# Kernel optimization log

Measured on AMD Instinct MI355X. Metric: run time of the kernel, lower is better.

Reference implementation:

```python
import jax, jax.numpy as jnp
import numpy as np

OUT, IN, GS = 4096, 4096, 128

def setup_inputs() -> dict:
    key = jax.random.key(0)
    k1, k2, k3 = jax.random.split(key, 3)
    x = jax.random.normal(k1, (2, 4096, IN), dtype=jnp.float32)
    # ternary codes in {-1, 0, 1}, stored as int8
    ternary = (jax.random.randint(k2, (OUT, IN), 0, 3) - 1).astype(jnp.int8)
    # per-group positive scales (one per contiguous group of GS weights)
    n_groups = OUT * IN // GS
    scales = jax.random.uniform(k3, (n_groups,), dtype=jnp.float32, minval=0.01, maxval=0.1)
    return {"x": x, "ternary": ternary, "scales": scales}

def reference(x, ternary, scales):
    # Reconstruct fp32 weight: each group of GS flattened weights shares one scale.
    w = (ternary.astype(jnp.float32).reshape(-1, GS) * scales[:, None]).reshape(OUT, IN)
    # F.linear: x @ W^T
    return jnp.einsum('bsi,oi->bso', x, w)
```

## Files before the change

### kernel.cpp

```cpp
#include <hip/hip_runtime.h>
#include <hip/hip_bf16.h>


#define M_DIM 8192
#define N_DIM 4096
#define K_DIM 4096
#define NGRP 32

#define BM 256
#define BN 256
#define NT 64
#define SLOT_B 16384
#define TILE_B 32768
#define A_BYTES (32ull * NT * TILE_B)
#define B_BYTES (16ull * NT * TILE_B)
#define A_CHUNKS (32 * 64 * 2 * 1024)
#define B_CHUNKS (16 * 64 * 2 * 1024)

typedef float f32x4 __attribute__((ext_vector_type(4)));
typedef float f32x16 __attribute__((ext_vector_type(16)));
typedef short bf16x8 __attribute__((ext_vector_type(8)));

__device__ __forceinline__ unsigned bfpack(unsigned lo, unsigned hi) {
  lo = (lo + 0x7FFFu + ((lo >> 16) & 1u)) >> 16;
  hi = (hi + 0x7FFFu + ((hi >> 16) & 1u)) & 0xFFFF0000u;
  return lo | hi;
}

__global__ void prep_ab(const float* __restrict__ X, const int* __restrict__ T,
                        const float* __restrict__ S, char* __restrict__ A,
                        char* __restrict__ B) {
  const int idx0 = blockIdx.x * blockDim.x + threadIdx.x;
  const int stride = gridDim.x * blockDim.x;
  for (int c = idx0; c < A_CHUNKS; c += stride) {
    int w = c & 1023, slot = c >> 10;
    int s = w >> 8, r = w & 255;
    int kk = slot & 1, kt = (slot >> 1) & 63, bm = slot >> 7;
    int gr = bm * 256 + r;
    int k0 = kt * 64 + kk * 32 + s * 8;
    const uint4* p = reinterpret_cast<const uint4*>(X + (size_t)gr * K_DIM + k0);
    uint4 u = p[0], v = p[1];
    uint4 o;
    o.x = bfpack(u.x, u.y);
    o.y = bfpack(u.z, u.w);
    o.z = bfpack(v.x, v.y);
    o.w = bfpack(v.z, v.w);
    *reinterpret_cast<uint4*>(A + (size_t)c * 16) = o;
  }
  for (int c = idx0; c < B_CHUNKS; c += stride) {
    int w = c & 1023, slot = c >> 10;
    int s = w >> 8, r = w & 255;
    int kk = slot & 1, kt = (slot >> 1) & 63, bn = slot >> 7;
    int gn = bn * 256 + r;
    int k0 = kt * 64 + kk * 32 + s * 8;
    unsigned su = __builtin_bit_cast(unsigned, S[(size_t)gn * NGRP + (kt >> 1)]);
    unsigned sb = (su + 0x7FFFu + ((su >> 16) & 1u)) >> 16;
    const int4* p = reinterpret_cast<const int4*>(T + (size_t)gn * K_DIM + k0);
    int4 u = p[0], v = p[1];
    int t0[8] = {u.x, u.y, u.z, u.w, v.x, v.y, v.z, v.w};
    unsigned h[8];
#pragma unroll
    for (int e = 0; e < 8; ++e) {
      unsigned sgn = ((unsigned)(t0[e] >> 31)) & 0x8000u;
      h[e] = t0[e] ? (sb | sgn) : 0u;
    }
    uint4 o;
    o.x = h[0] | (h[1] << 16);
    o.y = h[2] | (h[3] << 16);
    o.z = h[4] | (h[5] << 16);
    o.w = h[6] | (h[7] << 16);
    *reinterpret_cast<uint4*>(B + (size_t)c * 16) = o;
  }
}

__device__ __forceinline__ void gload16(const char* g, const char* l) {
  __builtin_amdgcn_global_load_lds(
      (const __attribute__((address_space(1))) void*)g,
      (__attribute__((address_space(3))) void*)l, 16, 0, 0);
}

__global__ __launch_bounds__(512, 2) void dqt_gemm32(
    const char* __restrict__ Aws, const char* __restrict__ Bws,
    float* __restrict__ C) {
  __shared__ __align__(16) char lds[131072];

  int b = blockIdx.x;
  int xcd = b & 7, idx = b >> 3;
  int bm = xcd * 4 + (idx >> 4);
  int bn = idx & 15;

  const int tid = threadIdx.x;
  const int lane = tid & 63;
  const int wid = tid >> 6;
  const int wr = wid >> 2;
  const int wc = wid & 3;
  const int l31 = lane & 31;
  const int lh = lane >> 5;

  const char* pA = Aws + ((size_t)bm << 21) + wid * 2048 + lane * 16;
  const char* pB = Bws + ((size_t)bn << 21) + wid * 2048 + lane * 16;
  const int sbase = wid * 2048;

#define STAGE(dstoff, src)                                \
  do {                                                    \
    gload16((src), lds + (dstoff) + sbase);               \
    gload16((src) + 1024, lds + (dstoff) + sbase + 1024); \
  } while (0)

  const int aoff = lh * 4096 + (wr * 128 + l31) * 16;
  const int boff = 32768 + lh * 4096 + (wc * 64 + l31) * 16;

  f32x16 acc[4][2] = {};

  STAGE(0, pA);
  STAGE(16384, pA + 16384);
  STAGE(32768, pB);
  STAGE(49152, pB + 16384);
  STAGE(65536, pA + 32768);
  STAGE(65536 + 32768, pB + 32768);
  asm volatile("s_waitcnt vmcnt(4)" ::: "memory");
  __builtin_amdgcn_s_barrier();

#pragma unroll 1
  for (int t = 0; t < NT; ++t) {
    const int cb = (t & 1) << 16;
    const int nb = (~t & 1) << 16;
    const char* sA1 = pA + (t + 1) * TILE_B;
    const char* sB1 = pB + (t + 1) * TILE_B;
    const char* sA2 = pA + (t + 2) * TILE_B;
    const char* sB2 = pB + (t + 2) * TILE_B;
    bf16x8 af[4], bq[2];

#pragma unroll
    for (int m = 0; m < 4; ++m)
      af[m] = *(const bf16x8*)(lds + cb + 0 + aoff + m * 512);
#pragma unroll
    for (int n = 0; n < 2; ++n)
      bq[n] = *(const bf16x8*)(lds + cb + 0 + boff + n * 512);
    if (t + 1 < NT) {
      STAGE(nb + 16384, sA1 + 16384);
      STAGE(nb + 49152, sB1 + 16384);
    }
    __builtin_amdgcn_s_barrier();
    __builtin_amdgcn_s_setprio(1);
#pragma unroll
    for (int m = 0; m < 4; ++m)
#pragma unroll
      for (int n = 0; n < 2; ++n)
        acc[m][n] = __builtin_amdgcn_mfma_f32_32x32x16_bf16(af[m], bq[n], acc[m][n], 0, 0, 0);
    __builtin_amdgcn_s_setprio(0);
    __builtin_amdgcn_s_barrier();

#pragma unroll
    for (int m = 0; m < 4; ++m)
      af[m] = *(const bf16x8*)(lds + cb + 8192 + aoff + m * 512);
#pragma unroll
    for (int n = 0; n < 2; ++n)
      bq[n] = *(const bf16x8*)(lds + cb + 8192 + boff + n * 512);
    __builtin_amdgcn_s_barrier();
    __builtin_amdgcn_s_setprio(1);
#pragma unroll
    for (int m = 0; m < 4; ++m)
#pragma unroll
      for (int n = 0; n < 2; ++n)
        acc[m][n] = __builtin_amdgcn_mfma_f32_32x32x16_bf16(af[m], bq[n], acc[m][n], 0, 0, 0);
    __builtin_amdgcn_s_setprio(0);
    __builtin_amdgcn_s_barrier();

#pragma unroll
    for (int m = 0; m < 4; ++m)
      af[m] = *(const bf16x8*)(lds + cb + 16384 + aoff + m * 512);
#pragma unroll
    for (int n = 0; n < 2; ++n)
      bq[n] = *(const bf16x8*)(lds + cb + 16384 + boff + n * 512);
    if (t + 2 < NT) STAGE(cb + 0, sA2);
    __builtin_amdgcn_s_barrier();
    __builtin_amdgcn_s_setprio(1);
#pragma unroll
    for (int m = 0; m < 4; ++m)
#pragma unroll
      for (int n = 0; n < 2; ++n)
        acc[m][n] = __builtin_amdgcn_mfma_f32_32x32x16_bf16(af[m], bq[n], acc[m][n], 0, 0, 0);
    __builtin_amdgcn_s_setprio(0);
    __builtin_amdgcn_s_barrier();

#pragma unroll
    for (int m = 0; m < 4; ++m)
      af[m] = *(const bf16x8*)(lds + cb + 16384 + 8192 + aoff + m * 512);
#pragma unroll
    for (int n = 0; n < 2; ++n)
      bq[n] = *(const bf16x8*)(lds + cb + 16384 + 8192 + boff + n * 512);
    if (t + 2 < NT) STAGE(cb + 32768, sB2);
    __builtin_amdgcn_s_barrier();
    __builtin_amdgcn_s_setprio(1);
#pragma unroll
    for (int m = 0; m < 4; ++m)
#pragma unroll
      for (int n = 0; n < 2; ++n)
        acc[m][n] = __builtin_amdgcn_mfma_f32_32x32x16_bf16(af[m], bq[n], acc[m][n], 0, 0, 0);
    __builtin_amdgcn_s_setprio(0);
    if (t < NT - 3)
      asm volatile("s_waitcnt vmcnt(4)" ::: "memory");
    else
      asm volatile("s_waitcnt vmcnt(0)" ::: "memory");
    __builtin_amdgcn_s_barrier();
  }

  const int row0 = bm * BM + wr * 128 + 4 * lh;
  const int col0 = bn * BN + wc * 64 + l31;
#pragma unroll
  for (int m = 0; m < 4; ++m)
#pragma unroll
    for (int n = 0; n < 2; ++n) {
      float* cp = C + (size_t)(row0 + m * 32) * N_DIM + col0 + n * 32;
#pragma unroll
      for (int q = 0; q < 16; ++q)
        cp[(size_t)((q & 3) + 8 * (q >> 2)) * N_DIM] = acc[m][n][q];
    }
#undef STAGE
}

struct StageRegs { float4 a0, a1, a2, a3; int4 b0, b1, b2, b3; float s; };

__device__ __forceinline__ void fb_issue(StageRegs& r, const float* __restrict__ X,
    const int* __restrict__ T, const float* __restrict__ S,
    int arow_g, int brow_g, int kt, int kq) {
  const int kbase = kt * 64;
  const float4* pa = reinterpret_cast<const float4*>(X + (size_t)arow_g * K_DIM + kbase + kq * 16);
  r.a0 = pa[0]; r.a1 = pa[1]; r.a2 = pa[2]; r.a3 = pa[3];
  const int4* pb = reinterpret_cast<const int4*>(T + (size_t)brow_g * K_DIM + kbase + kq * 16);
  r.b0 = pb[0]; r.b1 = pb[1]; r.b2 = pb[2]; r.b3 = pb[3];
  r.s = S[(size_t)brow_g * NGRP + (kt >> 1)];
}
__device__ __forceinline__ void fb_stage(const StageRegs& r, char* als, char* bls,
                                         int rrow, int kq) {
  const int xorv = (rrow & 7) << 4;
  const int base = rrow * 128 + kq * 32;
  const float* xf = (const float*)&r.a0;
  const int* wi = (const int*)&r.b0;
  bf16x8 av0, av1, wv0, wv1;
#pragma unroll
  for (int e = 0; e < 8; ++e) {
    av0[e] = __builtin_bit_cast(short, __float2bfloat16(xf[e]));
    av1[e] = __builtin_bit_cast(short, __float2bfloat16(xf[8 + e]));
    wv0[e] = __builtin_bit_cast(short, __float2bfloat16((float)wi[e] * r.s));
    wv1[e] = __builtin_bit_cast(short, __float2bfloat16((float)wi[8 + e] * r.s));
  }
  *(bf16x8*)(als + ((base) ^ xorv)) = av0;
  *(bf16x8*)(als + ((base + 16) ^ xorv)) = av1;
  *(bf16x8*)(bls + ((base) ^ xorv)) = wv0;
  *(bf16x8*)(bls + ((base + 16) ^ xorv)) = wv1;
}
__device__ __forceinline__ void fb_compute(const char* als, const char* bls,
    int lane, int wr, int wc, f32x4 (&acc)[4][2]) {
  const int lm = lane & 15;
  const int lk = (lane >> 4) << 4;
  const int xorv = (lm & 7) << 4;
#pragma unroll
  for (int ks = 0; ks < 2; ++ks) {
    const int kb = ks * 64 + lk;
    bf16x8 ah[4], bq[2];
#pragma unroll
    for (int i = 0; i < 4; ++i)
      ah[i] = *(const bf16x8*)(als + (((wr * 64 + i * 16 + lm) * 128 + kb) ^ xorv));
#pragma unroll
    for (int j = 0; j < 2; ++j)
      bq[j] = *(const bf16x8*)(bls + (((wc * 32 + j * 16 + lm) * 128 + kb) ^ xorv));
#pragma unroll
    for (int i = 0; i < 4; ++i)
#pragma unroll
      for (int j = 0; j < 2; ++j)
        acc[i][j] = __builtin_amdgcn_mfma_f32_16x16x32_bf16(ah[i], bq[j], acc[i][j], 0, 0, 0);
  }
}
__global__ __launch_bounds__(512, 2) void dqt_gemm_fb(
    const float* __restrict__ X, const int* __restrict__ T,
    const float* __restrict__ S, float* __restrict__ C) {
  int b = blockIdx.x;
  int wg = (b & 7) * 256 + (b >> 3);
  int bm = wg >> 5, bn = wg & 31;
  const int row0 = bm * 128, col0 = bn * 128;
  const int tid = threadIdx.x, lane = tid & 63, wid = tid >> 6;
  const int wr = wid >> 2, wc = wid & 3;
  __shared__ __align__(16) short lds_a[128 * 64];
  __shared__ __align__(16) short lds_b[128 * 64];
  char* als = (char*)lds_a;
  char* bls = (char*)lds_b;
  const int srow = tid >> 2, kq = tid & 3;
  const int arow_g = row0 + srow, brow_g = col0 + srow;
  f32x4 acc[4][2] = {};
  StageRegs rA, rB;
  fb_issue(rA, X, T, S, arow_g, brow_g, 0, kq);
#pragma unroll 1
  for (int p = 0; p < 32; ++p) {
    fb_stage(rA, als, bls, srow, kq);
    __syncthreads();
    fb_issue(rB, X, T, S, arow_g, brow_g, 2 * p + 1, kq);
    fb_compute(als, bls, lane, wr, wc, acc);
    __syncthreads();
    fb_stage(rB, als, bls, srow, kq);
    __syncthreads();
    if (p + 1 < 32) fb_issue(rA, X, T, S, arow_g, brow_g, 2 * p + 2, kq);
    fb_compute(als, bls, lane, wr, wc, acc);
    __syncthreads();
  }
  const int crow0 = row0 + wr * 64 + ((lane >> 4) << 2);
#pragma unroll
  for (int i = 0; i < 4; ++i)
#pragma unroll
    for (int j = 0; j < 2; ++j) {
      int colc = col0 + wc * 32 + j * 16 + (lane & 15);
#pragma unroll
      for (int q = 0; q < 4; ++q)
        C[(size_t)(crow0 + i * 16 + q) * N_DIM + colc] = acc[i][j][q];
    }
}

extern "C" void kernel_launch(void* const* d_in, const int* in_sizes, int n_in,
                              void* d_out, int out_size, void* d_ws, size_t ws_size,
                              hipStream_t stream) {
  const float* X = (const float*)d_in[0];
  const int* T = (const int*)d_in[1];
  const float* S = (const float*)d_in[2];
  float* C = (float*)d_out;
  if (ws_size >= A_BYTES + B_BYTES) {
    char* Aws = (char*)d_ws;
    char* Bws = (char*)d_ws + A_BYTES;
    prep_ab<<<2048, 256, 0, stream>>>(X, T, S, Aws, Bws);
    dqt_gemm32<<<512, 512, 0, stream>>>(Aws, Bws, C);
  } else {
    dqt_gemm_fb<<<2048, 512, 0, stream>>>(X, T, S, C);
  }
}
```

Baseline: 566.7 us.

## Tile prep kernel through LDS and halve GEMM barrier phases per k-tile

The prep kernel is rewritten so each workgroup converts one 256x64 tile of X or the ternary weights into LDS with an XOR swizzle, then writes it out contiguously. This replaces the old strided-per-chunk mapping with coalesced reads along K and fully contiguous writes. In the GEMM main loop, fragments for two k-substeps are loaded at once and the four compute phases per tile become two, with fewer barriers and both next-next stages issued together. The cost is more live VGPRs for the doubled fragment registers and a changed global-load issue pattern against the existing vmcnt waits.

```diff
diff --git a/kernel.cpp b/kernel.cpp
--- a/kernel.cpp
+++ b/kernel.cpp
@@ -10,12 +10,9 @@
 #define BM 256
 #define BN 256
 #define NT 64
-#define SLOT_B 16384
 #define TILE_B 32768
 #define A_BYTES (32ull * NT * TILE_B)
 #define B_BYTES (16ull * NT * TILE_B)
-#define A_CHUNKS (32 * 64 * 2 * 1024)
-#define B_CHUNKS (16 * 64 * 2 * 1024)
 
 typedef float f32x4 __attribute__((ext_vector_type(4)));
 typedef float f32x16 __attribute__((ext_vector_type(16)));
@@ -27,49 +24,77 @@
   return lo | hi;
 }
 
-__global__ void prep_ab(const float* __restrict__ X, const int* __restrict__ T,
-                        const float* __restrict__ S, char* __restrict__ A,
-                        char* __restrict__ B) {
-  const int idx0 = blockIdx.x * blockDim.x + threadIdx.x;
-  const int stride = gridDim.x * blockDim.x;
-  for (int c = idx0; c < A_CHUNKS; c += stride) {
-    int w = c & 1023, slot = c >> 10;
-    int s = w >> 8, r = w & 255;
-    int kk = slot & 1, kt = (slot >> 1) & 63, bm = slot >> 7;
-    int gr = bm * 256 + r;
-    int k0 = kt * 64 + kk * 32 + s * 8;
-    const uint4* p = reinterpret_cast<const uint4*>(X + (size_t)gr * K_DIM + k0);
-    uint4 u = p[0], v = p[1];
-    uint4 o;
-    o.x = bfpack(u.x, u.y);
-    o.y = bfpack(u.z, u.w);
-    o.z = bfpack(v.x, v.y);
-    o.w = bfpack(v.z, v.w);
-    *reinterpret_cast<uint4*>(A + (size_t)c * 16) = o;
-  }
-  for (int c = idx0; c < B_CHUNKS; c += stride) {
-    int w = c & 1023, slot = c >> 10;
-    int s = w >> 8, r = w & 255;
-    int kk = slot & 1, kt = (slot >> 1) & 63, bn = slot >> 7;
-    int gn = bn * 256 + r;
-    int k0 = kt * 64 + kk * 32 + s * 8;
-    unsigned su = __builtin_bit_cast(unsigned, S[(size_t)gn * NGRP + (kt >> 1)]);
-    unsigned sb = (su + 0x7FFFu + ((su >> 16) & 1u)) >> 16;
-    const int4* p = reinterpret_cast<const int4*>(T + (size_t)gn * K_DIM + k0);
-    int4 u = p[0], v = p[1];
-    int t0[8] = {u.x, u.y, u.z, u.w, v.x, v.y, v.z, v.w};
-    unsigned h[8];
-#pragma unroll
-    for (int e = 0; e < 8; ++e) {
-      unsigned sgn = ((unsigned)(t0[e] >> 31)) & 0x8000u;
-      h[e] = t0[e] ? (sb | sgn) : 0u;
-    }
-    uint4 o;
-    o.x = h[0] | (h[1] << 16);
-    o.y = h[2] | (h[3] << 16);
-    o.z = h[4] | (h[5] << 16);
-    o.w = h[6] | (h[7] << 16);
-    *reinterpret_cast<uint4*>(B + (size_t)c * 16) = o;
+__global__ __launch_bounds__(256) void prep_v2(
+    const float* __restrict__ X, const int* __restrict__ T,
+    const float* __restrict__ S, char* __restrict__ A, char* __restrict__ B) {
+  __shared__ __align__(16) char tile[32768];
+  const int t = threadIdx.x;
+  const int wg = blockIdx.x;
+
+  if (wg < 2048) {
+    const int a = wg >> 6, kt = wg & 63;
+    const float* src = X + ((size_t)a * 256) * K_DIM + kt * 64;
+#pragma unroll
+    for (int j = 0; j < 8; ++j) {
+      const int r = j * 32 + (t >> 3);
+      const int k8 = t & 7;
+      const uint4* p = reinterpret_cast<const uint4*>(src + (size_t)r * K_DIM + k8 * 8);
+      uint4 u = p[0], v = p[1];
+      uint4 o;
+      o.x = bfpack(u.x, u.y);
+      o.y = bfpack(u.z, u.w);
+      o.z = bfpack(v.x, v.y);
+      o.w = bfpack(v.z, v.w);
+      const int byte = ((k8 >> 2) << 14) + ((k8 & 3) << 12) + (r << 4);
+      *reinterpret_cast<uint4*>(tile + (byte ^ (k8 << 4))) = o;
+    }
+    __syncthreads();
+    char* dst = A + ((size_t)(a * 64 + kt) << 15);
+#pragma unroll
+    for (int j = 0; j < 8; ++j) {
+      const int lc = j * 256 + t;
+      uint4 d = *reinterpret_cast<const uint4*>(
+          tile + ((lc << 4) ^ (((lc >> 8) & 7) << 4)));
+      *reinterpret_cast<uint4*>(dst + (size_t)lc * 16) = d;
+    }
+  } else {
+    const int wgb = wg - 2048;
+    const int bn = wgb >> 6, kt = wgb & 63;
+    const int* src = T + ((size_t)bn * 256) * K_DIM + kt * 64;
+    const int grp = kt >> 1;
+#pragma unroll
+    for (int j = 0; j < 8; ++j) {
+      const int r = j * 32 + (t >> 3);
+      const int k8 = t & 7;
+      const int gn = bn * 256 + r;
+      unsigned su = __builtin_bit_cast(unsigned, S[(size_t)gn * NGRP + grp]);
+      unsigned sb = (su + 0x7FFFu + ((su >> 16) & 1u)) >> 16;
+      const int4* p = reinterpret_cast<const int4*>(src + (size_t)r * K_DIM + k8 * 8);
+      int4 u = p[0], v = p[1];
+      int tv[8] = {u.x, u.y, u.z, u.w, v.x, v.y, v.z, v.w};
+      unsigned h[8];
+#pragma unroll
+      for (int e = 0; e < 8; ++e) {
+        unsigned sgn = ((unsigned)(tv[e] >> 31)) & 0x8000u;
+        h[e] = tv[e] ? (sb | sgn) : 0u;
+      }
+      uint4 o;
+      o.x = h[0] | (h[1] << 16);
+      o.y = h[2] | (h[3] << 16);
+      o.z = h[4] | (h[5] << 16);
+      o.w = h[6] | (h[7] << 16);
+      const int byte = ((k8 >> 2) << 14) + ((k8 & 3) << 12) + (r << 4);
+      *reinterpret_cast<uint4*>(tile + (byte ^ (k8 << 4))) = o;
+    }
+    __syncthreads();
+    char* dst = B + ((size_t)(bn * 64 + kt) << 15);
+#pragma unroll
+    for (int j = 0; j < 8; ++j) {
+      const int lc = j * 256 + t;
+      uint4 d = *reinterpret_cast<const uint4*>(
+          tile + ((lc << 4) ^ (((lc >> 8) & 7) << 4)));
+      *reinterpret_cast<uint4*>(dst + (size_t)lc * 16) = d;
+    }
   }
 }
 
@@ -129,14 +154,18 @@
     const char* sB1 = pB + (t + 1) * TILE_B;
     const char* sA2 = pA + (t + 2) * TILE_B;
     const char* sB2 = pB + (t + 2) * TILE_B;
-    bf16x8 af[4], bq[2];
-
-#pragma unroll
-    for (int m = 0; m < 4; ++m)
-      af[m] = *(const bf16x8*)(lds + cb + 0 + aoff + m * 512);
-#pragma unroll
-    for (int n = 0; n < 2; ++n)
-      bq[n] = *(const bf16x8*)(lds + cb + 0 + boff + n * 512);
+    bf16x8 af0[4], af1[4], bq0[2], bq1[2];
+
+#pragma unroll
+    for (int m = 0; m < 4; ++m) {
+      af0[m] = *(const bf16x8*)(lds + cb + aoff + m * 512);
+      af1[m] = *(const bf16x8*)(lds + cb + 8192 + aoff + m * 512);
+    }
+#pragma unroll
+    for (int n = 0; n < 2; ++n) {
+      bq0[n] = *(const bf16x8*)(lds + cb + boff + n * 512);
+      bq1[n] = *(const bf16x8*)(lds + cb + 8192 + boff + n * 512);
+    }
     if (t + 1 < NT) {
       STAGE(nb + 16384, sA1 + 16384);
       STAGE(nb + 49152, sB1 + 16384);
@@ -147,57 +176,41 @@
     for (int m = 0; m < 4; ++m)
 #pragma unroll
       for (int n = 0; n < 2; ++n)
-        acc[m][n] = __builtin_amdgcn_mfma_f32_32x32x16_bf16(af[m], bq[n], acc[m][n], 0, 0, 0);
+        acc[m][n] = __builtin_amdgcn_mfma_f32_32x32x16_bf16(af0[m], bq0[n], acc[m][n], 0, 0, 0);
+#pragma unroll
+    for (int m = 0; m < 4; ++m)
+#pragma unroll
+      for (int n = 0; n < 2; ++n)
+        acc[m][n] = __builtin_amdgcn_mfma_f32_32x32x16_bf16(af1[m], bq1[n], acc[m][n], 0, 0, 0);
     __builtin_amdgcn_s_setprio(0);
     __builtin_amdgcn_s_barrier();
 
 #pragma unroll
-    for (int m = 0; m < 4; ++m)
-      af[m] = *(const bf16x8*)(lds + cb + 8192 + aoff + m * 512);
-#pragma unroll
-    for (int n = 0; n < 2; ++n)
-      bq[n] = *(const bf16x8*)(lds + cb + 8192 + boff + n * 512);
+    for (int m = 0; m < 4; ++m) {
+      af0[m] = *(const bf16x8*)(lds + cb + 16384 + aoff + m * 512);
+      af1[m] = *(const bf16x8*)(lds + cb + 16384 + 8192 + aoff + m * 512);
+    }
+#pragma unroll
+    for (int n = 0; n < 2; ++n) {
+      bq0[n] = *(const bf16x8*)(lds + cb + 16384 + boff + n * 512);
+      bq1[n] = *(const bf16x8*)(lds + cb + 16384 + 8192 + boff + n * 512);
+    }
+    if (t + 2 < NT) {
+      STAGE(cb + 0, sA2);
+      STAGE(cb + 32768, sB2);
+    }
     __builtin_amdgcn_s_barrier();
     __builtin_amdgcn_s_setprio(1);
 #pragma unroll
     for (int m = 0; m < 4; ++m)
 #pragma unroll
       for (int n = 0; n < 2; ++n)
-        acc[m][n] = __builtin_amdgcn_mfma_f32_32x32x16_bf16(af[m], bq[n], acc[m][n], 0, 0, 0);
-    __builtin_amdgcn_s_setprio(0);
-    __builtin_amdgcn_s_barrier();
-
+        acc[m][n] = __builtin_amdgcn_mfma_f32_32x32x16_bf16(af0[m], bq0[n], acc[m][n], 0, 0, 0);
 #pragma unroll
     for (int m = 0; m < 4; ++m)
-      af[m] = *(const bf16x8*)(lds + cb + 16384 + aoff + m * 512);
-#pragma unroll
-    for (int n = 0; n < 2; ++n)
-      bq[n] = *(const bf16x8*)(lds + cb + 16384 + boff + n * 512);
-    if (t + 2 < NT) STAGE(cb + 0, sA2);
-    __builtin_amdgcn_s_barrier();
-    __builtin_amdgcn_s_setprio(1);
-#pragma unroll
-    for (int m = 0; m < 4; ++m)
 #pragma unroll
       for (int n = 0; n < 2; ++n)
-        acc[m][n] = __builtin_amdgcn_mfma_f32_32x32x16_bf16(af[m], bq[n], acc[m][n], 0, 0, 0);
-    __builtin_amdgcn_s_setprio(0);
-    __builtin_amdgcn_s_barrier();
-
-#pragma unroll
-    for (int m = 0; m < 4; ++m)
-      af[m] = *(const bf16x8*)(lds + cb + 16384 + 8192 + aoff + m * 512);
-#pragma unroll
-    for (int n = 0; n < 2; ++n)
-      bq[n] = *(const bf16x8*)(lds + cb + 16384 + 8192 + boff + n * 512);
-    if (t + 2 < NT) STAGE(cb + 32768, sB2);
-    __builtin_amdgcn_s_barrier();
-    __builtin_amdgcn_s_setprio(1);
-#pragma unroll
-    for (int m = 0; m < 4; ++m)
-#pragma unroll
-      for (int n = 0; n < 2; ++n)
-        acc[m][n] = __builtin_amdgcn_mfma_f32_32x32x16_bf16(af[m], bq[n], acc[m][n], 0, 0, 0);
+        acc[m][n] = __builtin_amdgcn_mfma_f32_32x32x16_bf16(af1[m], bq1[n], acc[m][n], 0, 0, 0);
     __builtin_amdgcn_s_setprio(0);
     if (t < NT - 3)
       asm volatile("s_waitcnt vmcnt(4)" ::: "memory");
@@ -326,7 +339,7 @@
   if (ws_size >= A_BYTES + B_BYTES) {
     char* Aws = (char*)d_ws;
     char* Bws = (char*)d_ws + A_BYTES;
-    prep_ab<<<2048, 256, 0, stream>>>(X, T, S, Aws, Bws);
+    prep_v2<<<3072, 256, 0, stream>>>(X, T, S, Aws, Bws);
     dqt_gemm32<<<512, 512, 0, stream>>>(Aws, Bws, C);
   } else {
     dqt_gemm_fb<<<2048, 512, 0, stream>>>(X, T, S, C);
```

Result: faster. 512.5 us (-9.6%).
